# Kernel optimization log

Measured on AMD Instinct MI355X. Metric: run time of the kernel, lower is better.

Reference implementation:

```python
import jax, jax.numpy as jnp
import numpy as np

EPS = 1e-5
K = 32  # hardcoded k in SamplingGrouping.forward
S1, S2 = 512, 256  # samples


def conv_bn_relu(x, w, gamma, beta):
    # x: [B, C, L]; w: [O, C] (conv1d kernel_size=1, no bias)
    y = jnp.einsum('bcl,oc->bol', x, w)
    # BatchNorm1d in training mode: stats over (batch, length)
    mean = y.mean(axis=(0, 2), keepdims=True)
    var = y.var(axis=(0, 2), keepdims=True)
    yn = (y - mean) * jax.lax.rsqrt(var + EPS)
    return jax.nn.relu(yn * gamma[None, :, None] + beta[None, :, None])


def fps(coords, s):
    # Farthest point sampling; coords [B, N, 3] -> idx [B, s] (deterministic start at 0)
    B, N, _ = coords.shape
    init_idx = jnp.zeros((B,), jnp.int32)

    def body(carry, _):
        dist, last = carry
        p = jnp.take_along_axis(coords, last[:, None, None], axis=1)  # [B,1,3]
        d = jnp.sum((coords - p) ** 2, axis=-1)                        # [B,N]
        dist = jnp.minimum(dist, d)
        nxt = jnp.argmax(dist, axis=-1).astype(jnp.int32)
        return (dist, nxt), nxt

    (_, _), rest = jax.lax.scan(
        body, (jnp.full((B, N), 1e10, coords.dtype), init_idx), None, length=s - 1)
    return jnp.concatenate([init_idx[None, :], rest], axis=0).T  # [B, s]


def index_points(pts, idx):
    # pts [B,N,D], idx [B,...] int -> [B,...,D]
    return jax.vmap(lambda p, i: p[i])(pts, idx)


def sample_and_knn_group(s, k, coords, features):
    # coords [B,N,3], features [B,N,D] -> new_xyz [B,s,3], agg [B,s,k,2D]
    fps_idx = fps(coords, s)
    new_xyz = index_points(coords, fps_idx)      # [B,s,3]
    new_feat = index_points(features, fps_idx)   # [B,s,D]
    # squared distances [B,s,N]
    d = (jnp.sum(new_xyz ** 2, -1, keepdims=True)
         - 2.0 * jnp.einsum('bsc,bnc->bsn', new_xyz, coords)
         + jnp.sum(coords ** 2, -1)[:, None, :])
    _, knn_idx = jax.lax.top_k(-d, k)            # [B,s,k] nearest neighbours
    grouped = index_points(features, knn_idx)    # [B,s,k,D]
    grouped = grouped - new_feat[:, :, None, :]
    agg = jnp.concatenate(
        [grouped, jnp.broadcast_to(new_feat[:, :, None, :], grouped.shape)], axis=-1)
    return new_xyz, agg


def sg_block(s, coords, feats_bcn, wa, ga, ba, wb, gb, bb):
    # SamplingGrouping.forward
    feats = jnp.transpose(feats_bcn, (0, 2, 1))                 # [B,N,D]
    new_xyz, nf = sample_and_knn_group(s, K, coords, feats)     # [B,s,k,2D]
    b, s_, k, d = nf.shape
    nf = jnp.transpose(nf, (0, 1, 3, 2)).reshape(b * s_, d, k)  # [b*s, d, k]
    nf = conv_bn_relu(nf, wa, ga, ba)
    nf = conv_bn_relu(nf, wb, gb, bb)
    nf = nf.max(axis=2)                                         # adaptive_max_pool1d(.,1)
    nf = jnp.transpose(nf.reshape(b, s_, -1), (0, 2, 1))        # [b, O, s]
    return new_xyz, nf


def setup_inputs() -> dict:
    key = jax.random.key(0)
    ks = jax.random.split(key, 8)
    B, N = 32, 8192
    sc = 0.05
    inp = {
        'x': jax.random.normal(ks[0], (B, 3, N), jnp.float32),
        'w1': jax.random.normal(ks[1], (64, 3), jnp.float32) * sc,
        'g1': jnp.ones((64,), jnp.float32), 'b1': jnp.zeros((64,), jnp.float32),
        'w2': jax.random.normal(ks[2], (64, 64), jnp.float32) * sc,
        'g2': jnp.ones((64,), jnp.float32), 'b2': jnp.zeros((64,), jnp.float32),
        's1wa': jax.random.normal(ks[3], (128, 128), jnp.float32) * sc,
        's1ga': jnp.ones((128,), jnp.float32), 's1ba': jnp.zeros((128,), jnp.float32),
        's1wb': jax.random.normal(ks[4], (128, 128), jnp.float32) * sc,
        's1gb': jnp.ones((128,), jnp.float32), 's1bb': jnp.zeros((128,), jnp.float32),
        's2wa': jax.random.normal(ks[5], (256, 256), jnp.float32) * sc,
        's2ga': jnp.ones((256,), jnp.float32), 's2ba': jnp.zeros((256,), jnp.float32),
        's2wb': jax.random.normal(ks[6], (256, 256), jnp.float32) * sc,
        's2gb': jnp.ones((256,), jnp.float32), 's2bb': jnp.zeros((256,), jnp.float32),
    }
    return inp


def reference(x, w1, g1, b1, w2, g2, b2,
              s1wa, s1ga, s1ba, s1wb, s1gb, s1bb,
              s2wa, s2ga, s2ba, s2wb, s2gb, s2bb):
    xyz = jnp.transpose(x[:, :3, :], (0, 2, 1))  # [B,N,3]
    f = conv_bn_relu(x, w1, g1, b1)
    f = conv_bn_relu(f, w2, g2, b2)              # [B,64,N]
    xyz1, f1 = sg_block(S1, xyz, f, s1wa, s1ga, s1ba, s1wb, s1gb, s1bb)   # [B,128,S1]
    _, f2 = sg_block(S2, xyz1, f1, s2wa, s2ga, s2ba, s2wb, s2gb, s2bb)    # [B,256,S2]
    return f2
```

## Files before the change

kernel.cpp:

```cpp
#include <hip/hip_runtime.h>
#include <hip/hip_bf16.h>

#define NB 32
#define NP 8192

__device__ __forceinline__ float dist3(float ax, float ay, float az,
                                       float bx, float by, float bz) {
#pragma clang fp contract(off)
  float dx = ax - bx, dy = ay - by, dz = az - bz;
  return dx * dx + dy * dy + dz * dz;
}
__device__ __forceinline__ float sumsq3(float x, float y, float z) {
#pragma clang fp contract(off)
  return x * x + y * y + z * z;
}
__device__ __forceinline__ float knndist(float qx, float qy, float qz, float qq,
                                         float cx, float cy, float cz) {
#pragma clang fp contract(off)
  float dot = qx * cx + qy * cy + qz * cz;
  float cc = cx * cx + cy * cy + cz * cz;
  return (qq - 2.0f * dot) + cc;
}

__global__ void k_transpose(const float* __restrict__ w, float* __restrict__ wT,
                            int O, int Dd) {
  int i = blockIdx.x * 256 + threadIdx.x;
  if (i < O * Dd) {
    int o = i / Dd, d = i - o * Dd;
    wT[d * O + o] = w[i];
  }
}

__global__ void k_wdiff(const float* __restrict__ w, float* __restrict__ WdT,
                        int O, int D) {
  int i = blockIdx.x * 256 + threadIdx.x;
  if (i < D * O) {
    int d = i / O, o = i - d * O;
    WdT[i] = w[o * 2 * D + D + d] - w[o * 2 * D + d];
  }
}

__global__ __launch_bounds__(256) void k_s1a(const float* __restrict__ x,
                                             const float* __restrict__ w1,
                                             float* __restrict__ xyz,
                                             float* __restrict__ y1) {
  __shared__ float w1s[192];
  int t = threadIdx.x;
  if (t < 192) w1s[t] = w1[t];
  int gid = blockIdx.x * 256 + t;
  int b = gid >> 13, n = gid & (NP - 1);
  __syncthreads();
  const size_t xb = (size_t)b * 3 * NP;
  float x0 = x[xb + n], x1 = x[xb + NP + n], x2 = x[xb + 2 * NP + n];
  xyz[(size_t)gid * 3 + 0] = x0;
  xyz[(size_t)gid * 3 + 1] = x1;
  xyz[(size_t)gid * 3 + 2] = x2;
  float* yo = y1 + (size_t)gid * 64;
#pragma unroll
  for (int o = 0; o < 64; o += 4) {
    float4 v;
    v.x = x0 * w1s[(o + 0) * 3] + x1 * w1s[(o + 0) * 3 + 1] + x2 * w1s[(o + 0) * 3 + 2];
    v.y = x0 * w1s[(o + 1) * 3] + x1 * w1s[(o + 1) * 3 + 1] + x2 * w1s[(o + 1) * 3 + 2];
    v.z = x0 * w1s[(o + 2) * 3] + x1 * w1s[(o + 2) * 3 + 1] + x2 * w1s[(o + 2) * 3 + 2];
    v.w = x0 * w1s[(o + 3) * 3] + x1 * w1s[(o + 3) * 3 + 1] + x2 * w1s[(o + 3) * 3 + 2];
    *(float4*)&yo[o] = v;
  }
}

__global__ __launch_bounds__(256) void k_colstats(const float* __restrict__ buf,
                                                  size_t ME4, float* __restrict__ part) {
  __shared__ float red[128];
  int t = threadIdx.x;
  if (t < 128) red[t] = 0.f;
  float s[4] = {0.f, 0.f, 0.f, 0.f}, q[4] = {0.f, 0.f, 0.f, 0.f};
  size_t stride = (size_t)gridDim.x * 256;
  size_t i0 = (size_t)blockIdx.x * 256 + t;
  int c0 = (int)((i0 * 4) & 63);
  for (size_t i = i0; i < ME4; i += stride) {
    float4 v = ((const float4*)buf)[i];
    s[0] += v.x; q[0] += v.x * v.x;
    s[1] += v.y; q[1] += v.y * v.y;
    s[2] += v.z; q[2] += v.z * v.z;
    s[3] += v.w; q[3] += v.w * v.w;
  }
  __syncthreads();
#pragma unroll
  for (int j = 0; j < 4; ++j) {
    atomicAdd(&red[c0 + j], s[j]);
    atomicAdd(&red[64 + c0 + j], q[j]);
  }
  __syncthreads();
  if (t < 128) atomicAdd(&part[(size_t)(blockIdx.x & 63) * 128 + t], red[t]);
}

__global__ void k_bnfinal(const float* __restrict__ part, const float* __restrict__ gamma,
                          const float* __restrict__ beta, float invcnt, int C, int P,
                          float* __restrict__ sc) {
  int c = threadIdx.x;
  if (c >= C) return;
  float s = 0.f, q = 0.f;
  for (int p = 0; p < P; ++p) {
    s += part[(size_t)p * 2 * C + c];
    q += part[(size_t)p * 2 * C + C + c];
  }
  float mean = s * invcnt;
  float var = fmaxf(q * invcnt - mean * mean, 0.f);
  float scale = gamma[c] * rsqrtf(var + 1e-5f);
  sc[c] = scale;
  sc[C + c] = beta[c] - mean * scale;
}

__global__ __launch_bounds__(256) void k_s1c(const float* __restrict__ y1,
                                             const float* __restrict__ w2T,
                                             const float* __restrict__ sc1,
                                             float* __restrict__ y2) {
  __shared__ __align__(16) float f1[64 * 65];
  __shared__ __align__(16) float w2s[64 * 64];
  __shared__ float scs[128];
  int t = threadIdx.x;
  if (t < 128) scs[t] = sc1[t];
  for (int i = t; i < 4096; i += 256) w2s[i] = w2T[i];
  size_t base = (size_t)blockIdx.x * 4096;
  __syncthreads();
  for (int i = t; i < 4096; i += 256) {
    int p = i >> 6, c = i & 63;
    float v = y1[base + i];
    v = fmaxf(0.f, v * scs[c] + scs[64 + c]);
    f1[p * 65 + c] = v;
  }
  __syncthreads();
  int pq = t & 15, oq = t >> 4;
  int p0 = pq * 4, o0 = oq * 4;
  float ac[4][4] = {};
  for (int c = 0; c < 64; ++c) {
    float4 wv = *(const float4*)&w2s[c * 64 + o0];
    float a0 = f1[(p0 + 0) * 65 + c];
    float a1 = f1[(p0 + 1) * 65 + c];
    float a2 = f1[(p0 + 2) * 65 + c];
    float a3 = f1[(p0 + 3) * 65 + c];
    ac[0][0] += a0 * wv.x; ac[0][1] += a0 * wv.y; ac[0][2] += a0 * wv.z; ac[0][3] += a0 * wv.w;
    ac[1][0] += a1 * wv.x; ac[1][1] += a1 * wv.y; ac[1][2] += a1 * wv.z; ac[1][3] += a1 * wv.w;
    ac[2][0] += a2 * wv.x; ac[2][1] += a2 * wv.y; ac[2][2] += a2 * wv.z; ac[2][3] += a2 * wv.w;
    ac[3][0] += a3 * wv.x; ac[3][1] += a3 * wv.y; ac[3][2] += a3 * wv.z; ac[3][3] += a3 * wv.w;
  }
#pragma unroll
  for (int i2 = 0; i2 < 4; ++i2) {
    float4 v = {ac[i2][0], ac[i2][1], ac[i2][2], ac[i2][3]};
    *(float4*)&y2[base + (size_t)(p0 + i2) * 64 + o0] = v;
  }
}

__global__ __launch_bounds__(256) void k_s1e(float* __restrict__ y2,
                                             const float* __restrict__ sc2, size_t ME4) {
  __shared__ float scs[128];
  int t = threadIdx.x;
  if (t < 128) scs[t] = sc2[t];
  __syncthreads();
  size_t stride = (size_t)gridDim.x * 256;
  for (size_t i = (size_t)blockIdx.x * 256 + t; i < ME4; i += stride) {
    float4 v = ((float4*)y2)[i];
    int c0 = (int)((i * 4) & 63);
    v.x = fmaxf(0.f, v.x * scs[c0 + 0] + scs[64 + c0 + 0]);
    v.y = fmaxf(0.f, v.y * scs[c0 + 1] + scs[64 + c0 + 1]);
    v.z = fmaxf(0.f, v.z * scs[c0 + 2] + scs[64 + c0 + 2]);
    v.w = fmaxf(0.f, v.w * scs[c0 + 3] + scs[64 + c0 + 3]);
    ((float4*)y2)[i] = v;
  }
}

template <int N, int S, int PPT>
__global__ __launch_bounds__(N / PPT) void k_fps(const float* __restrict__ xyz,
                                                 int* __restrict__ fidx,
                                                 float* __restrict__ sxyz) {
  constexpr int T = N / PPT;
  constexpr int NW = T / 64;
  __shared__ float cl[N * 3];
  __shared__ float wv[2][NW];
  __shared__ int wi[2][NW];
  const int t = threadIdx.x;
  const int b = blockIdx.x;
  const float* base = xyz + (size_t)b * N * 3;
  for (int i = t; i < 3 * N; i += T) cl[i] = base[i];
  __syncthreads();
  float cx[PPT], cy[PPT], cz[PPT], dist[PPT];
#pragma unroll
  for (int j = 0; j < PPT; ++j) {
    int n = t + j * T;
    cx[j] = cl[n * 3 + 0];
    cy[j] = cl[n * 3 + 1];
    cz[j] = cl[n * 3 + 2];
    dist[j] = 1e10f;
  }
  float px = cl[0], py = cl[1], pz = cl[2];
  if (t == 0) {
    fidx[(size_t)b * S] = 0;
    sxyz[(size_t)b * S * 3 + 0] = px;
    sxyz[(size_t)b * S * 3 + 1] = py;
    sxyz[(size_t)b * S * 3 + 2] = pz;
  }
  int par = 0;
  for (int it = 1; it < S; ++it) {
    float bv = -1.0f;
    int bi = 0x7FFFFFFF;
#pragma unroll
    for (int j = 0; j < PPT; ++j) {
      float d = dist3(cx[j], cy[j], cz[j], px, py, pz);
      float dj = fminf(dist[j], d);
      dist[j] = dj;
      if (dj > bv) { bv = dj; bi = t + j * T; }
    }
#pragma unroll
    for (int off = 32; off > 0; off >>= 1) {
      float ov = __shfl_xor(bv, off);
      int oi = __shfl_xor(bi, off);
      if (ov > bv || (ov == bv && oi < bi)) { bv = ov; bi = oi; }
    }
    if ((t & 63) == 0) { wv[par][t >> 6] = bv; wi[par][t >> 6] = bi; }
    __syncthreads();
    float v = wv[par][0];
    int ii = wi[par][0];
#pragma unroll
    for (int w = 1; w < NW; ++w) {
      float ov = wv[par][w];
      int oi = wi[par][w];
      if (ov > v || (ov == v && oi < ii)) { v = ov; ii = oi; }
    }
    px = cl[ii * 3 + 0]; py = cl[ii * 3 + 1]; pz = cl[ii * 3 + 2];
    if (t == 0) {
      fidx[(size_t)b * S + it] = ii;
      sxyz[((size_t)b * S + it) * 3 + 0] = px;
      sxyz[((size_t)b * S + it) * 3 + 1] = py;
      sxyz[((size_t)b * S + it) * 3 + 2] = pz;
    }
    par ^= 1;
  }
}

template <int N, int S, int PPT>
__global__ __launch_bounds__(64) void k_fpsw(const float* __restrict__ xyz,
                                             int* __restrict__ fidx,
                                             float* __restrict__ sxyz) {
  __shared__ float cl[N * 3];
  const int t = threadIdx.x;
  const int b = blockIdx.x;
  const float* base = xyz + (size_t)b * N * 3;
  for (int i = t; i < 3 * N; i += 64) cl[i] = base[i];
  __syncthreads();
  float cx[PPT], cy[PPT], cz[PPT], dist[PPT];
#pragma unroll
  for (int j = 0; j < PPT; ++j) {
    int n = t + j * 64;
    cx[j] = cl[n * 3 + 0];
    cy[j] = cl[n * 3 + 1];
    cz[j] = cl[n * 3 + 2];
    dist[j] = 1e10f;
  }
  float px = cl[0], py = cl[1], pz = cl[2];
  if (t == 0) {
    fidx[(size_t)b * S] = 0;
    sxyz[(size_t)b * S * 3 + 0] = px;
    sxyz[(size_t)b * S * 3 + 1] = py;
    sxyz[(size_t)b * S * 3 + 2] = pz;
  }
  for (int it = 1; it < S; ++it) {
    float bv = -1.0f;
    int bi = 0x7FFFFFFF;
#pragma unroll
    for (int j = 0; j < PPT; ++j) {
      float d = dist3(cx[j], cy[j], cz[j], px, py, pz);
      float dj = fminf(dist[j], d);
      dist[j] = dj;
      if (dj > bv) { bv = dj; bi = t + j * 64; }
    }
#pragma unroll
    for (int off = 32; off > 0; off >>= 1) {
      float ov = __shfl_xor(bv, off);
      int oi = __shfl_xor(bi, off);
      if (ov > bv || (ov == bv && oi < bi)) { bv = ov; bi = oi; }
    }
    px = cl[bi * 3 + 0]; py = cl[bi * 3 + 1]; pz = cl[bi * 3 + 2];
    if (t == 0) {
      fidx[(size_t)b * S + it] = bi;
      sxyz[((size_t)b * S + it) * 3 + 0] = px;
      sxyz[((size_t)b * S + it) * 3 + 1] = py;
      sxyz[((size_t)b * S + it) * 3 + 2] = pz;
    }
  }
}

template <int NPT>
__global__ __launch_bounds__(256) void k_knn(const float* __restrict__ cxyz,
                                             const float* __restrict__ qxyz, int S,
                                             int* __restrict__ knn) {
  constexpr int N = NPT * 256;
  __shared__ float wv[2][4];
  __shared__ int wi[2][4];
  const int t = threadIdx.x;
  const int bs = blockIdx.x;
  const int b = bs / S;
  float qx = qxyz[(size_t)bs * 3 + 0];
  float qy = qxyz[(size_t)bs * 3 + 1];
  float qz = qxyz[(size_t)bs * 3 + 2];
  float qq = sumsq3(qx, qy, qz);
  const float* cb = cxyz + (size_t)b * N * 3;
  float ds[NPT];
  float lmin = 3.0e38f;
  int li = 0x7FFFFFFF;
#pragma unroll
  for (int j = 0; j < NPT; ++j) {
    int n = t + j * 256;
    float d = knndist(qx, qy, qz, qq, cb[(size_t)n * 3], cb[(size_t)n * 3 + 1],
                      cb[(size_t)n * 3 + 2]);
    ds[j] = d;
    if (d < lmin) { lmin = d; li = n; }
  }
  int par = 0;
  for (int r = 0; r < 32; ++r) {
    float bv = lmin;
    int bi = li;
#pragma unroll
    for (int off = 32; off > 0; off >>= 1) {
      float ov = __shfl_xor(bv, off);
      int oi = __shfl_xor(bi, off);
      if (ov < bv || (ov == bv && oi < bi)) { bv = ov; bi = oi; }
    }
    if ((t & 63) == 0) { wv[par][t >> 6] = bv; wi[par][t >> 6] = bi; }
    __syncthreads();
    float v = wv[par][0];
    int ii = wi[par][0];
#pragma unroll
    for (int w = 1; w < 4; ++w) {
      float ov = wv[par][w];
      int oi = wi[par][w];
      if (ov < v || (ov == v && oi < ii)) { v = ov; ii = oi; }
    }
    if (t == 0) knn[(size_t)bs * 32 + r] = ii;
    if (li == ii) {
#pragma unroll
      for (int j = 0; j < NPT; ++j)
        if (t + j * 256 == ii) ds[j] = 3.0e38f;
      lmin = 3.0e38f;
      li = 0x7FFFFFFF;
#pragma unroll
      for (int j = 0; j < NPT; ++j)
        if (ds[j] < lmin) { lmin = ds[j]; li = t + j * 256; }
    }
    par ^= 1;
  }
}

#define KP 36
__device__ __forceinline__ int swzcol(int d, int k) {
  return (k & 3) | ((((unsigned(k) >> 2) ^ (unsigned(d) >> 2)) & 7) << 2);
}

template <int DR, int O, int NT, int CH>
__device__ __forceinline__ void sg_gemm(const float* __restrict__ X,
                                        const float* __restrict__ WT,
                                        float* __restrict__ wch, int t, int o0, int kq,
                                        float (&ac)[4][4]) {
  for (int dc = 0; dc < DR; dc += CH) {
    __syncthreads();
    for (int i = t; i < CH * O; i += NT) wch[i] = WT[(size_t)dc * O + i];
    __syncthreads();
#pragma unroll 8
    for (int dd = 0; dd < CH; ++dd) {
      int d = dc + dd;
      const float4 wvv = *(const float4*)&wch[dd * O + o0];
      const float4 av = *(const float4*)&X[d * KP + ((kq ^ ((d >> 2) & 7)) << 2)];
      ac[0][0] += wvv.x * av.x; ac[0][1] += wvv.x * av.y; ac[0][2] += wvv.x * av.z; ac[0][3] += wvv.x * av.w;
      ac[1][0] += wvv.y * av.x; ac[1][1] += wvv.y * av.y; ac[1][2] += wvv.y * av.z; ac[1][3] += wvv.y * av.w;
      ac[2][0] += wvv.z * av.x; ac[2][1] += wvv.z * av.y; ac[2][2] += wvv.z * av.z; ac[2][3] += wvv.z * av.w;
      ac[3][0] += wvv.w * av.x; ac[3][1] += wvv.w * av.y; ac[3][2] += wvv.w * av.z; ac[3][3] += wvv.w * av.w;
    }
  }
}

template <int D, int NT>
__device__ __forceinline__ void sg_gatherV(const float* __restrict__ f, int Nf, int b,
                                           const int* __restrict__ nidx,
                                           float* __restrict__ V, int t) {
  constexpr int K = 32, DQ = D / 4;
  const float4* f4 = (const float4*)f;
  for (int idx = t; idx < K * DQ; idx += NT) {
    int k = idx / DQ, dq = idx - k * DQ;
    float4 v = f4[((size_t)b * Nf + nidx[k]) * DQ + dq];
    int d0 = dq * 4;
    V[(d0 + 0) * KP + swzcol(d0 + 0, k)] = v.x;
    V[(d0 + 1) * KP + swzcol(d0 + 1, k)] = v.y;
    V[(d0 + 2) * KP + swzcol(d0 + 2, k)] = v.z;
    V[(d0 + 3) * KP + swzcol(d0 + 3, k)] = v.w;
  }
}

template <int D, int O>
__device__ __forceinline__ void sg_corr(const float* __restrict__ WdT,
                                        const float* __restrict__ fqs, int o0, int kq,
                                        float (&c)[4]) {
  c[0] = c[1] = c[2] = c[3] = 0.f;
  for (int d = kq * (D / 8); d < (kq + 1) * (D / 8); ++d) {
    float qv = fqs[d];
    float4 wd = *(const float4*)&WdT[(size_t)d * O + o0];
    c[0] += wd.x * qv; c[1] += wd.y * qv; c[2] += wd.z * qv; c[3] += wd.w * qv;
  }
#pragma unroll
  for (int m = 1; m < 8; m <<= 1) {
    c[0] += __shfl_xor(c[0], m);
    c[1] += __shfl_xor(c[1], m);
    c[2] += __shfl_xor(c[2], m);
    c[3] += __shfl_xor(c[3], m);
  }
}

template <int D, int NT>
__global__ __launch_bounds__(NT) void k_sgA(const float* __restrict__ f, int Nf, int S,
                                            const int* __restrict__ fpsidx,
                                            const int* __restrict__ knn,
                                            const float* __restrict__ waT,
                                            const float* __restrict__ WdT,
                                            float* __restrict__ statsOut) {
  constexpr int D2 = 2 * D, O = D2, K = 32, CH = 16, DQ = D / 4;
  __shared__ __align__(16) float V[D * KP];
  __shared__ __align__(16) float wch[CH * O];
  __shared__ __align__(16) float fqs[D];
  __shared__ int nidx[K];
  __shared__ float red[2 * O];
  const int t = threadIdx.x;
  const int bs = blockIdx.x;
  const int b = bs / S;
  const int qi = fpsidx[bs];
  if (t < K) nidx[t] = knn[(size_t)bs * K + t];
  const float4* f4 = (const float4*)f;
  for (int i = t; i < DQ; i += NT)
    ((float4*)fqs)[i] = f4[((size_t)b * Nf + qi) * DQ + i];
  __syncthreads();
  sg_gatherV<D, NT>(f, Nf, b, nidx, V, t);
  const int oq = t >> 3, kq = t & 7;
  const int o0 = oq * 4;
  float c[4];
  sg_corr<D, O>(WdT, fqs, o0, kq, c);
  float acc[4][4];
#pragma unroll
  for (int i2 = 0; i2 < 4; ++i2)
#pragma unroll
    for (int j = 0; j < 4; ++j) acc[i2][j] = c[i2];
  sg_gemm<D, O, NT, CH>(V, waT, wch, t, o0, kq, acc);
#pragma unroll
  for (int i2 = 0; i2 < 4; ++i2) {
    float sv = acc[i2][0] + acc[i2][1] + acc[i2][2] + acc[i2][3];
    float sq = acc[i2][0] * acc[i2][0] + acc[i2][1] * acc[i2][1] +
               acc[i2][2] * acc[i2][2] + acc[i2][3] * acc[i2][3];
#pragma unroll
    for (int m = 1; m < 8; m <<= 1) {
      sv += __shfl_xor(sv, m);
      sq += __shfl_xor(sq, m);
    }
    if (kq == 0) {
      red[o0 + i2] = sv;
      red[O + o0 + i2] = sq;
    }
  }
  __syncthreads();
  float* slot = statsOut + (size_t)(bs & 255) * (2 * O);
  for (int i = t; i < 2 * O; i += NT) atomicAdd(&slot[i], red[i]);
}

template <int D, int NT>
__global__ __launch_bounds__(NT) void k_sgAB(const float* __restrict__ f, int Nf, int S,
                                             const int* __restrict__ fpsidx,
                                             const int* __restrict__ knn,
                                             const float* __restrict__ waT,
                                             const float* __restrict__ WdT,
                                             const float* __restrict__ wbT,
                                             const float* __restrict__ bnA,
                                             float* __restrict__ statsOut,
                                             float* __restrict__ mm) {
  constexpr int D2 = 2 * D, O = D2, K = 32, CH = 32, DQ = D / 4;
  __shared__ __align__(16) float VZ[O * KP];
  __shared__ __align__(16) float wch[CH * O];
  __shared__ __align__(16) float fqs[D];
  __shared__ int nidx[K];
  __shared__ float red[2 * O];
  __shared__ float scb[2 * O];
  const int t = threadIdx.x;
  const int bs = blockIdx.x;
  const int b = bs / S;
  const int qi = fpsidx[bs];
  if (t < K) nidx[t] = knn[(size_t)bs * K + t];
  const float4* f4 = (const float4*)f;
  for (int i = t; i < DQ; i += NT)
    ((float4*)fqs)[i] = f4[((size_t)b * Nf + qi) * DQ + i];
  for (int i = t; i < 2 * O; i += NT) scb[i] = bnA[i];
  __syncthreads();
  sg_gatherV<D, NT>(f, Nf, b, nidx, VZ, t);
  const int oq = t >> 3, kq = t & 7;
  const int o0 = oq * 4;
  float c[4];
  sg_corr<D, O>(WdT, fqs, o0, kq, c);
  float acc[4][4];
#pragma unroll
  for (int i2 = 0; i2 < 4; ++i2)
#pragma unroll
    for (int j = 0; j < 4; ++j) acc[i2][j] = c[i2];
  sg_gemm<D, O, NT, CH>(VZ, waT, wch, t, o0, kq, acc);
  __syncthreads();
#pragma unroll
  for (int i2 = 0; i2 < 4; ++i2) {
    float sA = scb[o0 + i2], tA = scb[O + o0 + i2];
    float4 z;
    z.x = fmaxf(0.f, acc[i2][0] * sA + tA);
    z.y = fmaxf(0.f, acc[i2][1] * sA + tA);
    z.z = fmaxf(0.f, acc[i2][2] * sA + tA);
    z.w = fmaxf(0.f, acc[i2][3] * sA + tA);
    *(float4*)&VZ[(o0 + i2) * KP + ((kq ^ (oq & 7)) << 2)] = z;
  }
  float ac2[4][4];
#pragma unroll
  for (int i2 = 0; i2 < 4; ++i2)
#pragma unroll
    for (int j = 0; j < 4; ++j) ac2[i2][j] = 0.f;
  sg_gemm<O, O, NT, CH>(VZ, wbT, wch, t, o0, kq, ac2);
  float* mrow = mm + (size_t)bs * 2 * O;
#pragma unroll
  for (int i2 = 0; i2 < 4; ++i2) {
    float sv = ac2[i2][0] + ac2[i2][1] + ac2[i2][2] + ac2[i2][3];
    float sq = ac2[i2][0] * ac2[i2][0] + ac2[i2][1] * ac2[i2][1] +
               ac2[i2][2] * ac2[i2][2] + ac2[i2][3] * ac2[i2][3];
    float mx = fmaxf(fmaxf(ac2[i2][0], ac2[i2][1]), fmaxf(ac2[i2][2], ac2[i2][3]));
    float mn = fminf(fminf(ac2[i2][0], ac2[i2][1]), fminf(ac2[i2][2], ac2[i2][3]));
#pragma unroll
    for (int m = 1; m < 8; m <<= 1) {
      sv += __shfl_xor(sv, m);
      sq += __shfl_xor(sq, m);
      mx = fmaxf(mx, __shfl_xor(mx, m));
      mn = fminf(mn, __shfl_xor(mn, m));
    }
    if (kq == 0) {
      red[o0 + i2] = sv;
      red[O + o0 + i2] = sq;
      mrow[o0 + i2] = mx;
      mrow[O + o0 + i2] = mn;
    }
  }
  __syncthreads();
  float* slot = statsOut + (size_t)(bs & 255) * (2 * O);
  for (int i = t; i < 2 * O; i += NT) atomicAdd(&slot[i], red[i]);
}

template <int O>
__global__ __launch_bounds__(256) void k_fin(const float* __restrict__ mm,
                                             const float* __restrict__ bnB, int S,
                                             float* __restrict__ out, int finalOut) {
  int idx = blockIdx.x * 256 + threadIdx.x;
  int o, bs;
  if (finalOut) {
    int s = idx % S;
    int bo = idx / S;
    o = bo % O;
    int b = bo / O;
    bs = b * S + s;
  } else {
    o = idx % O;
    bs = idx / O;
  }
  float sB = bnB[o], tB = bnB[O + o];
  const float* r = mm + (size_t)bs * 2 * O;
  float ext = (sB >= 0.f) ? r[o] : r[O + o];
  out[idx] = fmaxf(0.f, sB * ext + tB);
}

extern "C" void kernel_launch(void* const* d_in, const int* in_sizes, int n_in,
                              void* d_out, int out_size, void* d_ws, size_t ws_size,
                              hipStream_t stream) {
  (void)in_sizes; (void)n_in; (void)out_size; (void)ws_size;
  const float* x    = (const float*)d_in[0];
  const float* w1   = (const float*)d_in[1];
  const float* g1   = (const float*)d_in[2];
  const float* b1   = (const float*)d_in[3];
  const float* w2   = (const float*)d_in[4];
  const float* g2   = (const float*)d_in[5];
  const float* b2   = (const float*)d_in[6];
  const float* s1wa = (const float*)d_in[7];
  const float* s1ga = (const float*)d_in[8];
  const float* s1ba = (const float*)d_in[9];
  const float* s1wb = (const float*)d_in[10];
  const float* s1gb = (const float*)d_in[11];
  const float* s1bb = (const float*)d_in[12];
  const float* s2wa = (const float*)d_in[13];
  const float* s2ga = (const float*)d_in[14];
  const float* s2ba = (const float*)d_in[15];
  const float* s2wb = (const float*)d_in[16];
  const float* s2gb = (const float*)d_in[17];
  const float* s2bb = (const float*)d_in[18];
  float* out = (float*)d_out;

  char* wsp = (char*)d_ws;
  size_t off = 0;
  auto alloc = [&](size_t floats) {
    void* p = wsp + off;
    off += ((floats * 4 + 255) & ~(size_t)255);
    return p;
  };
  float* xyz  = (float*)alloc(786432);
  float* y1   = (float*)alloc(16777216);
  float* y2f  = y1;
  float* f1f  = (float*)alloc(2097152);
  float* xyz1 = (float*)alloc(49152);
  float* xyz2 = (float*)alloc(24576);
  int* fi1    = (int*)alloc(16384);
  int* fi2    = (int*)alloc(8192);
  int* kn1    = (int*)alloc(524288);
  int* kn2    = (int*)alloc(262144);
  float* w2T  = (float*)alloc(4096);
  float* waT1 = (float*)alloc(16384);
  float* wbT1 = (float*)alloc(16384);
  float* waT2 = (float*)alloc(65536);
  float* wbT2 = (float*)alloc(65536);
  float* WdT1 = (float*)alloc(8192);
  float* WdT2 = (float*)alloc(32768);
  float* stats = (float*)alloc(411392);
  float* part_s1 = stats;
  float* part_s2 = stats + 8192;
  float* partA1  = stats + 16384;
  float* partB1  = stats + 81920;
  float* partA2  = stats + 147456;
  float* partB2  = stats + 278528;
  float* sc1  = stats + 409600;
  float* sc2  = sc1 + 128;
  float* bnA1 = sc2 + 128;
  float* bnB1 = bnA1 + 256;
  float* bnA2 = bnB1 + 256;
  float* bnB2 = bnA2 + 512;
  float* mm = (float*)alloc(4194304);

  hipMemsetAsync(stats, 0, (size_t)409600 * 4, stream);

  k_transpose<<<(64 * 64 + 255) / 256, 256, 0, stream>>>(w2, w2T, 64, 64);
  k_transpose<<<(128 * 128 + 255) / 256, 256, 0, stream>>>(s1wa, waT1, 128, 128);
  k_transpose<<<(128 * 128 + 255) / 256, 256, 0, stream>>>(s1wb, wbT1, 128, 128);
  k_transpose<<<(256 * 256 + 255) / 256, 256, 0, stream>>>(s2wa, waT2, 256, 256);
  k_transpose<<<(256 * 256 + 255) / 256, 256, 0, stream>>>(s2wb, wbT2, 256, 256);
  k_wdiff<<<(64 * 128 + 255) / 256, 256, 0, stream>>>(s1wa, WdT1, 128, 64);
  k_wdiff<<<(128 * 256 + 255) / 256, 256, 0, stream>>>(s2wa, WdT2, 256, 128);

  const size_t MN = (size_t)NB * NP;
  k_s1a<<<(int)(MN / 256), 256, 0, stream>>>(x, w1, xyz, y1);
  k_colstats<<<1024, 256, 0, stream>>>(y1, MN * 16, part_s1);
  k_bnfinal<<<1, 64, 0, stream>>>(part_s1, g1, b1, 1.f / (float)MN, 64, 64, sc1);
  k_s1c<<<(int)(MN / 64), 256, 0, stream>>>(y1, w2T, sc1, y2f);
  k_colstats<<<1024, 256, 0, stream>>>(y2f, MN * 16, part_s2);
  k_bnfinal<<<1, 64, 0, stream>>>(part_s2, g2, b2, 1.f / (float)MN, 64, 64, sc2);
  k_s1e<<<2048, 256, 0, stream>>>(y2f, sc2, MN * 16);

  k_fps<NP, 512, 32><<<NB, 256, 0, stream>>>(xyz, fi1, xyz1);
  k_knn<32><<<NB * 512, 256, 0, stream>>>(xyz, xyz1, 512, kn1);

  const float icA1 = 1.f / (32.f * 512.f * 32.f);
  const float icA2 = 1.f / (32.f * 256.f * 32.f);

  k_sgA<64, 256><<<NB * 512, 256, 0, stream>>>(y2f, NP, 512, fi1, kn1, waT1, WdT1, partA1);
  k_bnfinal<<<1, 128, 0, stream>>>(partA1, s1ga, s1ba, icA1, 128, 256, bnA1);
  k_sgAB<64, 256><<<NB * 512, 256, 0, stream>>>(y2f, NP, 512, fi1, kn1, waT1, WdT1,
                                                wbT1, bnA1, partB1, mm);
  k_bnfinal<<<1, 128, 0, stream>>>(partB1, s1gb, s1bb, icA1, 128, 256, bnB1);
  k_fin<128><<<8192, 256, 0, stream>>>(mm, bnB1, 512, f1f, 0);

  k_fpsw<512, 256, 8><<<NB, 64, 0, stream>>>(xyz1, fi2, xyz2);
  k_knn<2><<<NB * 256, 256, 0, stream>>>(xyz1, xyz2, 256, kn2);

  k_sgA<128, 512><<<NB * 256, 512, 0, stream>>>(f1f, 512, 256, fi2, kn2, waT2, WdT2, partA2);
  k_bnfinal<<<1, 256, 0, stream>>>(partA2, s2ga, s2ba, icA2, 256, 256, bnA2);
  k_sgAB<128, 512><<<NB * 256, 512, 0, stream>>>(f1f, 512, 256, fi2, kn2, waT2, WdT2,
                                                 wbT2, bnA2, partB2, mm);
  k_bnfinal<<<1, 256, 0, stream>>>(partB2, s2gb, s2bb, icA2, 256, 256, bnB2);
  k_fin<256><<<8192, 256, 0, stream>>>(mm, bnB2, 256, out, 1);
}
```

Baseline: 4.253 ms.

## Split GEMM reduction across two thread halves with 8x4 register tiles and prefetch

The per-group GEMMs in the sampling-grouping kernels now give each thread an 8-output by 4-neighbour register tile instead of 4x4. The reduction dimension is split between two halves of the block, and their partial sums are combined through shared memory. Weight chunks are prefetched into registers one step ahead, so the global load overlaps compute. The aim is more FMAs per shared-memory load and hidden global latency, at the cost of more registers, extra barriers for the combine step, and idle threads during the epilogue.

```diff
diff --git a/kernel.cpp b/kernel.cpp
--- a/kernel.cpp
+++ b/kernel.cpp
@@ -354,28 +354,6 @@
   return (k & 3) | ((((unsigned(k) >> 2) ^ (unsigned(d) >> 2)) & 7) << 2);
 }
 
-template <int DR, int O, int NT, int CH>
-__device__ __forceinline__ void sg_gemm(const float* __restrict__ X,
-                                        const float* __restrict__ WT,
-                                        float* __restrict__ wch, int t, int o0, int kq,
-                                        float (&ac)[4][4]) {
-  for (int dc = 0; dc < DR; dc += CH) {
-    __syncthreads();
-    for (int i = t; i < CH * O; i += NT) wch[i] = WT[(size_t)dc * O + i];
-    __syncthreads();
-#pragma unroll 8
-    for (int dd = 0; dd < CH; ++dd) {
-      int d = dc + dd;
-      const float4 wvv = *(const float4*)&wch[dd * O + o0];
-      const float4 av = *(const float4*)&X[d * KP + ((kq ^ ((d >> 2) & 7)) << 2)];
-      ac[0][0] += wvv.x * av.x; ac[0][1] += wvv.x * av.y; ac[0][2] += wvv.x * av.z; ac[0][3] += wvv.x * av.w;
-      ac[1][0] += wvv.y * av.x; ac[1][1] += wvv.y * av.y; ac[1][2] += wvv.y * av.z; ac[1][3] += wvv.y * av.w;
-      ac[2][0] += wvv.z * av.x; ac[2][1] += wvv.z * av.y; ac[2][2] += wvv.z * av.z; ac[2][3] += wvv.z * av.w;
-      ac[3][0] += wvv.w * av.x; ac[3][1] += wvv.w * av.y; ac[3][2] += wvv.w * av.z; ac[3][3] += wvv.w * av.w;
-    }
-  }
-}
-
 template <int D, int NT>
 __device__ __forceinline__ void sg_gatherV(const float* __restrict__ f, int Nf, int b,
                                            const int* __restrict__ nidx,
@@ -393,33 +371,106 @@
   }
 }
 
+template <int DR, int O, int NT, int CH>
+__device__ __forceinline__ void sg_gemm8(const float* __restrict__ X,
+                                         const float* __restrict__ WT,
+                                         float* __restrict__ wch, int t, int o0,
+                                         int kq, int g, float (&ac)[8][4]) {
+  constexpr int HR = DR / 2, HC = CH / 2, NCH = DR / CH;
+  constexpr int PF = (CH * O) / (NT * 4);
+  float4 pf[PF];
+#pragma unroll
+  for (int q = 0; q < PF; ++q) {
+    int fidx = (t + q * NT) * 4;
+    int r = fidx / O, cc = fidx - r * O;
+    int gr = (r < HC) ? r : (HR - HC + r);
+    pf[q] = *(const float4*)&WT[(size_t)gr * O + cc];
+  }
+  const int dbase0 = g * HR, wbase = g * HC;
+  for (int c = 0; c < NCH; ++c) {
+    __syncthreads();
+#pragma unroll
+    for (int q = 0; q < PF; ++q) *(float4*)&wch[(t + q * NT) * 4] = pf[q];
+    __syncthreads();
+    if (c + 1 < NCH) {
+#pragma unroll
+      for (int q = 0; q < PF; ++q) {
+        int fidx = (t + q * NT) * 4;
+        int r = fidx / O, cc = fidx - r * O;
+        int gr = (r < HC) ? ((c + 1) * HC + r) : (HR + (c + 1) * HC + (r - HC));
+        pf[q] = *(const float4*)&WT[(size_t)gr * O + cc];
+      }
+    }
+    const int dbase = dbase0 + c * HC;
+#pragma unroll
+    for (int dd = 0; dd < HC; ++dd) {
+      int d = dbase + dd;
+      const float4 av = *(const float4*)&X[d * KP + ((kq ^ ((d >> 2) & 7)) << 2)];
+      const float4 w0 = *(const float4*)&wch[(wbase + dd) * O + o0];
+      const float4 w1 = *(const float4*)&wch[(wbase + dd) * O + o0 + 4];
+      ac[0][0] += w0.x*av.x; ac[0][1] += w0.x*av.y; ac[0][2] += w0.x*av.z; ac[0][3] += w0.x*av.w;
+      ac[1][0] += w0.y*av.x; ac[1][1] += w0.y*av.y; ac[1][2] += w0.y*av.z; ac[1][3] += w0.y*av.w;
+      ac[2][0] += w0.z*av.x; ac[2][1] += w0.z*av.y; ac[2][2] += w0.z*av.z; ac[2][3] += w0.z*av.w;
+      ac[3][0] += w0.w*av.x; ac[3][1] += w0.w*av.y; ac[3][2] += w0.w*av.z; ac[3][3] += w0.w*av.w;
+      ac[4][0] += w1.x*av.x; ac[4][1] += w1.x*av.y; ac[4][2] += w1.x*av.z; ac[4][3] += w1.x*av.w;
+      ac[5][0] += w1.y*av.x; ac[5][1] += w1.y*av.y; ac[5][2] += w1.y*av.z; ac[5][3] += w1.y*av.w;
+      ac[6][0] += w1.z*av.x; ac[6][1] += w1.z*av.y; ac[6][2] += w1.z*av.z; ac[6][3] += w1.z*av.w;
+      ac[7][0] += w1.w*av.x; ac[7][1] += w1.w*av.y; ac[7][2] += w1.w*av.z; ac[7][3] += w1.w*av.w;
+    }
+  }
+}
+
+template <int NT>
+__device__ __forceinline__ void sg_combine(float* __restrict__ wch, int tid2, int g,
+                                           float (&ac)[8][4]) {
+  constexpr int NH = NT / 2;
+#pragma unroll
+  for (int h = 0; h < 2; ++h) {
+    __syncthreads();
+    if (g == 1) {
+#pragma unroll
+      for (int i = 0; i < 4; ++i)
+        *(float4*)&wch[(i * NH + tid2) * 4] = *(float4*)&ac[h * 4 + i][0];
+    }
+    __syncthreads();
+    if (g == 0) {
+#pragma unroll
+      for (int i = 0; i < 4; ++i) {
+        float4 v = *(const float4*)&wch[(i * NH + tid2) * 4];
+        ac[h*4+i][0] += v.x; ac[h*4+i][1] += v.y; ac[h*4+i][2] += v.z; ac[h*4+i][3] += v.w;
+      }
+    }
+  }
+}
+
 template <int D, int O>
-__device__ __forceinline__ void sg_corr(const float* __restrict__ WdT,
-                                        const float* __restrict__ fqs, int o0, int kq,
-                                        float (&c)[4]) {
-  c[0] = c[1] = c[2] = c[3] = 0.f;
+__device__ __forceinline__ void sg_corr8(const float* __restrict__ WdT,
+                                         const float* __restrict__ fqs, int o0, int kq,
+                                         float (&c)[8]) {
+#pragma unroll
+  for (int i = 0; i < 8; ++i) c[i] = 0.f;
   for (int d = kq * (D / 8); d < (kq + 1) * (D / 8); ++d) {
     float qv = fqs[d];
-    float4 wd = *(const float4*)&WdT[(size_t)d * O + o0];
-    c[0] += wd.x * qv; c[1] += wd.y * qv; c[2] += wd.z * qv; c[3] += wd.w * qv;
+    float4 w0 = *(const float4*)&WdT[(size_t)d * O + o0];
+    float4 w1 = *(const float4*)&WdT[(size_t)d * O + o0 + 4];
+    c[0] += w0.x * qv; c[1] += w0.y * qv; c[2] += w0.z * qv; c[3] += w0.w * qv;
+    c[4] += w1.x * qv; c[5] += w1.y * qv; c[6] += w1.z * qv; c[7] += w1.w * qv;
   }
 #pragma unroll
   for (int m = 1; m < 8; m <<= 1) {
-    c[0] += __shfl_xor(c[0], m);
-    c[1] += __shfl_xor(c[1], m);
-    c[2] += __shfl_xor(c[2], m);
-    c[3] += __shfl_xor(c[3], m);
-  }
-}
-
-template <int D, int NT>
+#pragma unroll
+    for (int i = 0; i < 8; ++i) c[i] += __shfl_xor(c[i], m);
+  }
+}
+
+template <int D, int NT, int CH>
 __global__ __launch_bounds__(NT) void k_sgA(const float* __restrict__ f, int Nf, int S,
                                             const int* __restrict__ fpsidx,
                                             const int* __restrict__ knn,
                                             const float* __restrict__ waT,
                                             const float* __restrict__ WdT,
                                             float* __restrict__ statsOut) {
-  constexpr int D2 = 2 * D, O = D2, K = 32, CH = 16, DQ = D / 4;
+  constexpr int D2 = 2 * D, O = D2, K = 32, DQ = D / 4;
   __shared__ __align__(16) float V[D * KP];
   __shared__ __align__(16) float wch[CH * O];
   __shared__ __align__(16) float fqs[D];
@@ -435,29 +486,35 @@
     ((float4*)fqs)[i] = f4[((size_t)b * Nf + qi) * DQ + i];
   __syncthreads();
   sg_gatherV<D, NT>(f, Nf, b, nidx, V, t);
-  const int oq = t >> 3, kq = t & 7;
-  const int o0 = oq * 4;
-  float c[4];
-  sg_corr<D, O>(WdT, fqs, o0, kq, c);
-  float acc[4][4];
-#pragma unroll
-  for (int i2 = 0; i2 < 4; ++i2)
-#pragma unroll
-    for (int j = 0; j < 4; ++j) acc[i2][j] = c[i2];
-  sg_gemm<D, O, NT, CH>(V, waT, wch, t, o0, kq, acc);
-#pragma unroll
-  for (int i2 = 0; i2 < 4; ++i2) {
-    float sv = acc[i2][0] + acc[i2][1] + acc[i2][2] + acc[i2][3];
-    float sq = acc[i2][0] * acc[i2][0] + acc[i2][1] * acc[i2][1] +
-               acc[i2][2] * acc[i2][2] + acc[i2][3] * acc[i2][3];
-#pragma unroll
-    for (int m = 1; m < 8; m <<= 1) {
-      sv += __shfl_xor(sv, m);
-      sq += __shfl_xor(sq, m);
-    }
-    if (kq == 0) {
-      red[o0 + i2] = sv;
-      red[O + o0 + i2] = sq;
+  const int tid2 = t & (NT / 2 - 1);
+  const int g = t >= (NT / 2);
+  const int kq = tid2 & 7;
+  const int o0 = (tid2 >> 3) * 8;
+  float ac[8][4];
+#pragma unroll
+  for (int i = 0; i < 8; ++i)
+#pragma unroll
+    for (int j = 0; j < 4; ++j) ac[i][j] = 0.f;
+  sg_gemm8<D, O, NT, CH>(V, waT, wch, t, o0, kq, g, ac);
+  sg_combine<NT>(wch, tid2, g, ac);
+  if (g == 0) {
+    float c8[8];
+    sg_corr8<D, O>(WdT, fqs, o0, kq, c8);
+#pragma unroll
+    for (int i = 0; i < 8; ++i) {
+      float a0 = ac[i][0] + c8[i], a1 = ac[i][1] + c8[i];
+      float a2 = ac[i][2] + c8[i], a3 = ac[i][3] + c8[i];
+      float sv = a0 + a1 + a2 + a3;
+      float sq = a0 * a0 + a1 * a1 + a2 * a2 + a3 * a3;
+#pragma unroll
+      for (int m = 1; m < 8; m <<= 1) {
+        sv += __shfl_xor(sv, m);
+        sq += __shfl_xor(sq, m);
+      }
+      if (kq == 0) {
+        red[o0 + i] = sv;
+        red[O + o0 + i] = sq;
+      }
     }
   }
   __syncthreads();
@@ -465,7 +522,7 @@
   for (int i = t; i < 2 * O; i += NT) atomicAdd(&slot[i], red[i]);
 }
 
-template <int D, int NT>
+template <int D, int NT, int CH>
 __global__ __launch_bounds__(NT) void k_sgAB(const float* __restrict__ f, int Nf, int S,
                                              const int* __restrict__ fpsidx,
                                              const int* __restrict__ knn,
@@ -475,7 +532,7 @@
                                              const float* __restrict__ bnA,
                                              float* __restrict__ statsOut,
                                              float* __restrict__ mm) {
-  constexpr int D2 = 2 * D, O = D2, K = 32, CH = 32, DQ = D / 4;
+  constexpr int D2 = 2 * D, O = D2, K = 32, DQ = D / 4;
   __shared__ __align__(16) float VZ[O * KP];
   __shared__ __align__(16) float wch[CH * O];
   __shared__ __align__(16) float fqs[D];
@@ -493,53 +550,61 @@
   for (int i = t; i < 2 * O; i += NT) scb[i] = bnA[i];
   __syncthreads();
   sg_gatherV<D, NT>(f, Nf, b, nidx, VZ, t);
-  const int oq = t >> 3, kq = t & 7;
-  const int o0 = oq * 4;
-  float c[4];
-  sg_corr<D, O>(WdT, fqs, o0, kq, c);
-  float acc[4][4];
-#pragma unroll
-  for (int i2 = 0; i2 < 4; ++i2)
-#pragma unroll
-    for (int j = 0; j < 4; ++j) acc[i2][j] = c[i2];
-  sg_gemm<D, O, NT, CH>(VZ, waT, wch, t, o0, kq, acc);
-  __syncthreads();
-#pragma unroll
-  for (int i2 = 0; i2 < 4; ++i2) {
-    float sA = scb[o0 + i2], tA = scb[O + o0 + i2];
-    float4 z;
-    z.x = fmaxf(0.f, acc[i2][0] * sA + tA);
-    z.y = fmaxf(0.f, acc[i2][1] * sA + tA);
-    z.z = fmaxf(0.f, acc[i2][2] * sA + tA);
-    z.w = fmaxf(0.f, acc[i2][3] * sA + tA);
-    *(float4*)&VZ[(o0 + i2) * KP + ((kq ^ (oq & 7)) << 2)] = z;
-  }
-  float ac2[4][4];
-#pragma unroll
-  for (int i2 = 0; i2 < 4; ++i2)
-#pragma unroll
-    for (int j = 0; j < 4; ++j) ac2[i2][j] = 0.f;
-  sg_gemm<O, O, NT, CH>(VZ, wbT, wch, t, o0, kq, ac2);
+  const int tid2 = t & (NT / 2 - 1);
+  const int g = t >= (NT / 2);
+  const int kq = tid2 & 7;
+  const int o0 = (tid2 >> 3) * 8;
+  float ac[8][4];
+#pragma unroll
+  for (int i = 0; i < 8; ++i)
+#pragma unroll
+    for (int j = 0; j < 4; ++j) ac[i][j] = 0.f;
+  sg_gemm8<D, O, NT, CH>(VZ, waT, wch, t, o0, kq, g, ac);
+  sg_combine<NT>(wch, tid2, g, ac);
+  if (g == 0) {
+    float c8[8];
+    sg_corr8<D, O>(WdT, fqs, o0, kq, c8);
+#pragma unroll
+    for (int i = 0; i < 8; ++i) {
+      int o = o0 + i;
+      float sA = scb[o], tA = scb[O + o];
+      float4 z;
+      z.x = fmaxf(0.f, (ac[i][0] + c8[i]) * sA + tA);
+      z.y = fmaxf(0.f, (ac[i][1] + c8[i]) * sA + tA);
+      z.z = fmaxf(0.f, (ac[i][2] + c8[i]) * sA + tA);
+      z.w = fmaxf(0.f, (ac[i][3] + c8[i]) * sA + tA);
+      *(float4*)&VZ[o * KP + ((kq ^ ((o >> 2) & 7)) << 2)] = z;
+    }
+  }
+  float ac2[8][4];
+#pragma unroll
+  for (int i = 0; i < 8; ++i)
+#pragma unroll
+    for (int j = 0; j < 4; ++j) ac2[i][j] = 0.f;
+  sg_gemm8<O, O, NT, CH>(VZ, wbT, wch, t, o0, kq, g, ac2);
+  sg_combine<NT>(wch, tid2, g, ac2);
   float* mrow = mm + (size_t)bs * 2 * O;
-#pragma unroll
-  for (int i2 = 0; i2 < 4; ++i2) {
-    float sv = ac2[i2][0] + ac2[i2][1] + ac2[i2][2] + ac2[i2][3];
-    float sq = ac2[i2][0] * ac2[i2][0] + ac2[i2][1] * ac2[i2][1] +
-               ac2[i2][2] * ac2[i2][2] + ac2[i2][3] * ac2[i2][3];
-    float mx = fmaxf(fmaxf(ac2[i2][0], ac2[i2][1]), fmaxf(ac2[i2][2], ac2[i2][3]));
-    float mn = fminf(fminf(ac2[i2][0], ac2[i2][1]), fminf(ac2[i2][2], ac2[i2][3]));
-#pragma unroll
-    for (int m = 1; m < 8; m <<= 1) {
-      sv += __shfl_xor(sv, m);
-      sq += __shfl_xor(sq, m);
-      mx = fmaxf(mx, __shfl_xor(mx, m));
-      mn = fminf(mn, __shfl_xor(mn, m));
-    }
-    if (kq == 0) {
-      red[o0 + i2] = sv;
-      red[O + o0 + i2] = sq;
-      mrow[o0 + i2] = mx;
-      mrow[O + o0 + i2] = mn;
+  if (g == 0) {
+#pragma unroll
+    for (int i = 0; i < 8; ++i) {
+      float a0 = ac2[i][0], a1 = ac2[i][1], a2 = ac2[i][2], a3 = ac2[i][3];
+      float sv = a0 + a1 + a2 + a3;
+      float sq = a0 * a0 + a1 * a1 + a2 * a2 + a3 * a3;
+      float mx = fmaxf(fmaxf(a0, a1), fmaxf(a2, a3));
+      float mn = fminf(fminf(a0, a1), fminf(a2, a3));
+#pragma unroll
+      for (int m = 1; m < 8; m <<= 1) {
+        sv += __shfl_xor(sv, m);
+        sq += __shfl_xor(sq, m);
+        mx = fmaxf(mx, __shfl_xor(mx, m));
+        mn = fminf(mn, __shfl_xor(mn, m));
+      }
+      if (kq == 0) {
+        red[o0 + i] = sv;
+        red[O + o0 + i] = sq;
+        mrow[o0 + i] = mx;
+        mrow[O + o0 + i] = mn;
+      }
     }
   }
   __syncthreads();
@@ -658,20 +723,22 @@
   const float icA1 = 1.f / (32.f * 512.f * 32.f);
   const float icA2 = 1.f / (32.f * 256.f * 32.f);
 
-  k_sgA<64, 256><<<NB * 512, 256, 0, stream>>>(y2f, NP, 512, fi1, kn1, waT1, WdT1, partA1);
+  k_sgA<64, 256, 16><<<NB * 512, 256, 0, stream>>>(y2f, NP, 512, fi1, kn1, waT1, WdT1,
+                                                   partA1);
   k_bnfinal<<<1, 128, 0, stream>>>(partA1, s1ga, s1ba, icA1, 128, 256, bnA1);
-  k_sgAB<64, 256><<<NB * 512, 256, 0, stream>>>(y2f, NP, 512, fi1, kn1, waT1, WdT1,
-                                                wbT1, bnA1, partB1, mm);
+  k_sgAB<64, 256, 32><<<NB * 512, 256, 0, stream>>>(y2f, NP, 512, fi1, kn1, waT1, WdT1,
+                                                    wbT1, bnA1, partB1, mm);
   k_bnfinal<<<1, 128, 0, stream>>>(partB1, s1gb, s1bb, icA1, 128, 256, bnB1);
   k_fin<128><<<8192, 256, 0, stream>>>(mm, bnB1, 512, f1f, 0);
 
   k_fpsw<512, 256, 8><<<NB, 64, 0, stream>>>(xyz1, fi2, xyz2);
   k_knn<2><<<NB * 256, 256, 0, stream>>>(xyz1, xyz2, 256, kn2);
 
-  k_sgA<128, 512><<<NB * 256, 512, 0, stream>>>(f1f, 512, 256, fi2, kn2, waT2, WdT2, partA2);
+  k_sgA<128, 512, 16><<<NB * 256, 512, 0, stream>>>(f1f, 512, 256, fi2, kn2, waT2, WdT2,
+                                                    partA2);
   k_bnfinal<<<1, 256, 0, stream>>>(partA2, s2ga, s2ba, icA2, 256, 256, bnA2);
-  k_sgAB<128, 512><<<NB * 256, 512, 0, stream>>>(f1f, 512, 256, fi2, kn2, waT2, WdT2,
-                                                 wbT2, bnA2, partB2, mm);
+  k_sgAB<128, 512, 32><<<NB * 256, 512, 0, stream>>>(f1f, 512, 256, fi2, kn2, waT2, WdT2,
+                                                     wbT2, bnA2, partB2, mm);
   k_bnfinal<<<1, 256, 0, stream>>>(partB2, s2gb, s2bb, icA2, 256, 256, bnB2);
   k_fin<256><<<8192, 256, 0, stream>>>(mm, bnB2, 256, out, 1);
 }
```

After: 5.891 ms. 1.39x slower.
